# Kernel tuning notes

Hardware: AMD Instinct MI355X
Metric: run time of the kernel (lower is better)

## Reference

```python
import jax, jax.numpy as jnp
import numpy as np

K_SIZE = 32768   # knowledge_size
H = 1024         # hidden_size
Q = 512          # query_dim


def setup_inputs() -> dict:
    key = jax.random.key(0)
    kq, kb_, kwk, kbk, kwv, kbv = jax.random.split(key, 6)
    queries = jax.random.normal(kq, (4, 2048, Q), dtype=jnp.float32)
    knowledge_bank = jax.random.normal(kb_, (K_SIZE, H), dtype=jnp.float32)
    # Linear layers: torch Linear weight [out, in]; we store transposed [in, out]
    lim_k = 1.0 / np.sqrt(H)
    Wk = jax.random.uniform(kwk, (H, Q), jnp.float32, -lim_k, lim_k)
    bk = jax.random.uniform(kbk, (Q,), jnp.float32, -lim_k, lim_k)
    Wv = jax.random.uniform(kwv, (H, H), jnp.float32, -lim_k, lim_k)
    bv = jax.random.uniform(kbv, (H,), jnp.float32, -lim_k, lim_k)
    return {"queries": queries, "knowledge_bank": knowledge_bank,
            "Wk": Wk, "bk": bk, "Wv": Wv, "bv": bv}


def reference(queries, knowledge_bank, Wk, bk, Wv, bv):
    # keys: [K, Q]
    knowledge_keys = knowledge_bank @ Wk + bk
    # scores: [B, S, K]  (note: original applies NO 1/sqrt(d) scaling)
    scores = jnp.einsum('bsq,kq->bsk', queries, knowledge_keys)
    attention = jax.nn.softmax(scores, axis=-1)
    # values: [K, H]
    knowledge_values = knowledge_bank @ Wv + bv
    # retrieved: [B, S, H]
    return jnp.einsum('bsk,kh->bsh', attention, knowledge_values)
```

## Files before the change

### kernel.cpp

```cpp
#include <hip/hip_runtime.h>
#include <cstdint>
#include <cstddef>


typedef __bf16 bf16_t;
typedef __bf16 bf16x4 __attribute__((ext_vector_type(4)));
typedef __bf16 bf16x8 __attribute__((ext_vector_type(8)));
typedef _Float16 f16_t;
typedef _Float16 f16x4 __attribute__((ext_vector_type(4)));
typedef _Float16 f16x8 __attribute__((ext_vector_type(8)));
typedef float f32x4 __attribute__((ext_vector_type(4)));

#define KS   32768
#define HDIM 1024
#define QDIM 512
#define NQ   8192
#define SOFTMAX_C 90.0f

__device__ __forceinline__ void async16(const void* g, void* l) {
  __builtin_amdgcn_global_load_lds((const __attribute__((address_space(1))) void*)g,
                                   (__attribute__((address_space(3))) void*)l, 16, 0, 0);
}

__device__ __forceinline__ void barrier_f() {
  asm volatile("" ::: "memory");
  __builtin_amdgcn_s_barrier();
  asm volatile("" ::: "memory");
}

template <typename T>
__device__ __forceinline__ void stage_tile(const T* gbase, size_t ld, int k0,
                                           T* lds, int wave, int lane) {
  const int gp = ((lane & 3) ^ ((lane >> 3) & 3)) * 8;
  for (int c = wave; c < 8; c += 4) {
    const T* g = gbase + (size_t)(c * 16 + (lane >> 2)) * ld + (size_t)k0 + gp;
    async16((const void*)g, (void*)(lds + c * 512));
  }
}

template <typename T>
__device__ __forceinline__ void stage_half(const T* gbase, size_t ld, int gk,
                                           T* ldsbase, int wave, int lane) {
#pragma unroll
  for (int g = 0; g < 2; ++g) {
    const int slot = g * 512 + wave * 64 + lane;
    const int row = slot >> 2;
    const int cx = (slot & 3) ^ ((row >> 1) & 3);
    const T* src = gbase + (size_t)row * ld + (size_t)gk + cx * 8;
    async16((const void*)src, (void*)(ldsbase + g * 4096 + wave * 512));
  }
}

struct MF16 {
  typedef f16_t T; typedef f16x8 V8;
  static __device__ __forceinline__ f32x4 mm(V8 a, V8 b, f32x4 c) {
    return __builtin_amdgcn_mfma_f32_16x16x32_f16(a, b, c, 0, 0, 0);
  }
};
struct MBF16 {
  typedef bf16_t T; typedef bf16x8 V8;
  static __device__ __forceinline__ f32x4 mm(V8 a, V8 b, f32x4 c) {
    return __builtin_amdgcn_mfma_f32_16x16x32_bf16(a, b, c, 0, 0, 0);
  }
};

template <class M>
__device__ __forceinline__ void gemm256_8p(
    const typename M::T* __restrict__ A, size_t lda,
    const typename M::T* __restrict__ B, size_t ldb,
    int kbeg, int ktiles, typename M::T* sm,
    f32x4 (&acc)[8][4], int wave, int lane) {
  typedef typename M::T T;
  typedef typename M::V8 V8;
  const int wm = wave & 1, wn = wave >> 1;
  const int qd = lane >> 4, ln = lane & 15;
  const int arow = wm * 128 + ln;
  const int brow = wn * 64 + ln;
  const int cxr = (qd ^ ((ln >> 1) & 3)) * 8;

  stage_half(B, ldb, kbeg +  0, sm + 16384, wave, lane);
  stage_half(B, ldb, kbeg + 32, sm + 24576, wave, lane);
  stage_half(A, lda, kbeg +  0, sm +     0, wave, lane);
  stage_half(A, lda, kbeg + 32, sm +  8192, wave, lane);
  stage_half(B, ldb, kbeg + 64, sm + 32768 + 16384, wave, lane);
  stage_half(B, ldb, kbeg + 96, sm + 32768 + 24576, wave, lane);
  stage_half(A, lda, kbeg + 64, sm + 32768, wave, lane);
  asm volatile("s_waitcnt vmcnt(6)" ::: "memory");
  barrier_f();

  V8 ar[4], br0[4], br1[4];
  for (int t = 0; t < ktiles; ++t) {
    const int b = t & 1;
    T* bufA = sm + b * 32768;
    T* bufB = bufA + 16384;
    T* obufA = sm + (b ^ 1) * 32768;
    const int kt = kbeg + t * 64;
#pragma unroll
    for (int j = 0; j < 4; ++j) br0[j] = *(const V8*)&bufB[(brow + j * 16) * 32 + cxr];
#pragma unroll
    for (int i = 0; i < 4; ++i) ar[i] = *(const V8*)&bufA[(arow + i * 16) * 32 + cxr];
    if (t + 1 < ktiles) stage_half(A, lda, kt + 96, obufA + 8192, wave, lane);
    barrier_f();
    asm volatile("s_waitcnt lgkmcnt(0)" ::: "memory");
    __builtin_amdgcn_s_setprio(1);
#pragma unroll
    for (int i = 0; i < 4; ++i)
#pragma unroll
      for (int j = 0; j < 4; ++j) acc[i][j] = M::mm(ar[i], br0[j], acc[i][j]);
    __builtin_amdgcn_s_setprio(0);
    barrier_f();
#pragma unroll
    for (int j = 0; j < 4; ++j) br1[j] = *(const V8*)&bufB[8192 + (brow + j * 16) * 32 + cxr];
#pragma unroll
    for (int i = 0; i < 4; ++i) ar[i] = *(const V8*)&bufA[8192 + (arow + i * 16) * 32 + cxr];
    if (t + 2 < ktiles) stage_half(B, ldb, kt + 128, bufB, wave, lane);
    barrier_f();
    asm volatile("s_waitcnt lgkmcnt(0)" ::: "memory");
    __builtin_amdgcn_s_setprio(1);
#pragma unroll
    for (int i = 0; i < 4; ++i)
#pragma unroll
      for (int j = 0; j < 4; ++j) acc[i][j] = M::mm(ar[i], br1[j], acc[i][j]);
    __builtin_amdgcn_s_setprio(0);
    barrier_f();
#pragma unroll
    for (int i = 0; i < 4; ++i) ar[i] = *(const V8*)&bufA[(arow + 64 + i * 16) * 32 + cxr];
    if (t + 2 < ktiles) stage_half(B, ldb, kt + 160, bufB + 8192, wave, lane);
    barrier_f();
    asm volatile("s_waitcnt lgkmcnt(0)" ::: "memory");
    __builtin_amdgcn_s_setprio(1);
#pragma unroll
    for (int i = 0; i < 4; ++i)
#pragma unroll
      for (int j = 0; j < 4; ++j) acc[4 + i][j] = M::mm(ar[i], br0[j], acc[4 + i][j]);
    __builtin_amdgcn_s_setprio(0);
    barrier_f();
#pragma unroll
    for (int i = 0; i < 4; ++i) ar[i] = *(const V8*)&bufA[8192 + (arow + 64 + i * 16) * 32 + cxr];
    if (t + 2 < ktiles) stage_half(A, lda, kt + 128, bufA, wave, lane);
    barrier_f();
    asm volatile("s_waitcnt lgkmcnt(0)" ::: "memory");
    __builtin_amdgcn_s_setprio(1);
#pragma unroll
    for (int i = 0; i < 4; ++i)
#pragma unroll
      for (int j = 0; j < 4; ++j) acc[4 + i][j] = M::mm(ar[i], br1[j], acc[4 + i][j]);
    __builtin_amdgcn_s_setprio(0);
    if (t + 2 < ktiles) { asm volatile("s_waitcnt vmcnt(6)" ::: "memory"); }
    else                { asm volatile("s_waitcnt vmcnt(0)" ::: "memory"); }
    barrier_f();
  }
}

__global__ __launch_bounds__(256) void prep_q(const float* __restrict__ q,
                                              f16_t* __restrict__ qf) {
  int g = blockIdx.x * 256 + threadIdx.x;
  float4 v = *(const float4*)(q + (size_t)g * 4);
  f16x4 h;
  h[0] = (f16_t)v.x; h[1] = (f16_t)v.y; h[2] = (f16_t)v.z; h[3] = (f16_t)v.w;
  *(f16x4*)(qf + (size_t)g * 4) = h;
}

__global__ __launch_bounds__(256) void prep_bank(const float* __restrict__ bank,
                                                 f16_t* __restrict__ bh,
                                                 bf16_t* __restrict__ bb) {
  size_t g = (size_t)blockIdx.x * 256 + threadIdx.x;
  float4 v = *(const float4*)(bank + g * 4);
  f16x4 h;
  h[0] = (f16_t)v.x; h[1] = (f16_t)v.y; h[2] = (f16_t)v.z; h[3] = (f16_t)v.w;
  *(f16x4*)(bh + g * 4) = h;
  bf16x4 b;
  b[0] = (bf16_t)v.x; b[1] = (bf16_t)v.y; b[2] = (bf16_t)v.z; b[3] = (bf16_t)v.w;
  *(bf16x4*)(bb + g * 4) = b;
}

__global__ __launch_bounds__(256) void prep_wk(const float* __restrict__ Wk,
                                               f16_t* __restrict__ WkTf) {
  int t = blockIdx.x * 256 + threadIdx.x;
  int n = t >> 10, k = t & 1023;
  WkTf[t] = (f16_t)Wk[(size_t)k * QDIM + n];
}

__global__ __launch_bounds__(256) void prep_wv(const float* __restrict__ Wv,
                                               bf16_t* __restrict__ WvT) {
  int t = blockIdx.x * 256 + threadIdx.x;
  int n = t >> 10, k = t & 1023;
  WvT[t] = (bf16_t)(Wv[(size_t)k * HDIM + n]);
}

__global__ __launch_bounds__(256) void keys_gemm(const f16_t* __restrict__ bh,
                                                 const f16_t* __restrict__ WkTf,
                                                 const float* __restrict__ bk,
                                                 f16_t* __restrict__ kf) {
  __shared__ alignas(16) f16_t lA[128 * 32];
  __shared__ alignas(16) f16_t lB[128 * 32];
  const int tid = threadIdx.x, lane = tid & 63, wave = tid >> 6;
  const int wm = wave & 1, wn = wave >> 1;
  const int qd = lane >> 4, ln = lane & 15;
  const int m0 = blockIdx.y * 128;
  const int n0 = blockIdx.x * 128;
  const int kqs = ((qd ^ ((ln >> 1) & 3)) << 3);
  f32x4 acc[4][4] = {};
  for (int k0 = 0; k0 < HDIM; k0 += 32) {
    stage_tile(bh + (size_t)m0 * HDIM, HDIM, k0, lA, wave, lane);
    stage_tile(WkTf + (size_t)n0 * HDIM, HDIM, k0, lB, wave, lane);
    __syncthreads();
    f16x8 af[4], bfr[4];
#pragma unroll
    for (int i = 0; i < 4; i++)
      af[i] = *(const f16x8*)&lA[(wm * 64 + i * 16 + ln) * 32 + kqs];
#pragma unroll
    for (int j = 0; j < 4; j++)
      bfr[j] = *(const f16x8*)&lB[(wn * 64 + j * 16 + ln) * 32 + kqs];
#pragma unroll
    for (int i = 0; i < 4; i++)
#pragma unroll
      for (int j = 0; j < 4; j++)
        acc[i][j] = __builtin_amdgcn_mfma_f32_16x16x32_f16(af[i], bfr[j], acc[i][j], 0, 0, 0);
    __syncthreads();
  }
#pragma unroll
  for (int j = 0; j < 4; j++) {
    const int cc = n0 + wn * 64 + j * 16 + ln;
    const float bkc = bk[cc];
#pragma unroll
    for (int i = 0; i < 4; i++) {
      const int rr = m0 + wm * 64 + i * 16 + qd * 4;
#pragma unroll
      for (int r = 0; r < 4; r++)
        kf[(size_t)(rr + r) * QDIM + cc] = (f16_t)(acc[i][j][r] + bkc);
    }
  }
}

__global__ __launch_bounds__(256) void values_gemm_t(const bf16_t* __restrict__ bb,
                                                     const bf16_t* __restrict__ WvT,
                                                     const float* __restrict__ bv,
                                                     bf16_t* __restrict__ VT) {
  __shared__ alignas(16) bf16_t lA[128 * 32];
  __shared__ alignas(16) bf16_t lB[128 * 32];
  const int tid = threadIdx.x, lane = tid & 63, wave = tid >> 6;
  const int wm = wave & 1, wn = wave >> 1;
  const int qd = lane >> 4, ln = lane & 15;
  const int m0 = blockIdx.x * 128;
  const int n0 = blockIdx.y * 128;
  const int kqs = ((qd ^ ((ln >> 1) & 3)) << 3);
  f32x4 acc[4][4] = {};
  for (int k0 = 0; k0 < HDIM; k0 += 32) {
    stage_tile(WvT + (size_t)m0 * HDIM, HDIM, k0, lA, wave, lane);
    stage_tile(bb + (size_t)n0 * HDIM, HDIM, k0, lB, wave, lane);
    __syncthreads();
    bf16x8 af[4], bfr[4];
#pragma unroll
    for (int i = 0; i < 4; i++)
      af[i] = *(const bf16x8*)&lA[(wm * 64 + i * 16 + ln) * 32 + kqs];
#pragma unroll
    for (int j = 0; j < 4; j++)
      bfr[j] = *(const bf16x8*)&lB[(wn * 64 + j * 16 + ln) * 32 + kqs];
#pragma unroll
    for (int i = 0; i < 4; i++)
#pragma unroll
      for (int j = 0; j < 4; j++)
        acc[i][j] = __builtin_amdgcn_mfma_f32_16x16x32_bf16(af[i], bfr[j], acc[i][j], 0, 0, 0);
    __syncthreads();
  }
#pragma unroll
  for (int i = 0; i < 4; i++) {
#pragma unroll
    for (int r = 0; r < 4; r++) {
      const int hh = m0 + wm * 64 + i * 16 + qd * 4 + r;
      const float bvc = bv[hh];
#pragma unroll
      for (int j = 0; j < 4; j++) {
        const int cc = n0 + wn * 64 + j * 16 + ln;
        VT[(size_t)hh * KS + cc] = (bf16_t)(acc[i][j][r] + bvc);
      }
    }
  }
}

__global__ __launch_bounds__(512, 2) void score_fused_8p(
    const f16_t* __restrict__ qf, const f16_t* __restrict__ kf,
    bf16_t* __restrict__ P, float* __restrict__ lpart, int row0, int mtiles) {
  __shared__ alignas(16) f16_t sm[65536];
  const int tid = threadIdx.x, lane = tid & 63, wave = tid >> 6;
  const int bid = blockIdx.x;
  const int logical = (bid & 7) * ((int)gridDim.x >> 3) + (bid >> 3);
  const int mt_ = logical % mtiles;
  const int nt_ = logical / mtiles;
  const int m0 = mt_ * 256, n0 = nt_ * 256;
  f32x4 acc[8][4] = {};
  gemm256_8p<MF16>(qf + (size_t)(row0 + m0) * QDIM, QDIM,
                   kf + (size_t)n0 * QDIM, QDIM, 0, QDIM / 64, sm, acc, wave, lane);

  const int wm = wave & 1, wn = wave >> 1;
  const int qd = lane >> 4, ln = lane & 15;
  float* ls = (float*)sm;
  if (tid < 256) ls[tid] = 0.f;
  __syncthreads();
  float rsum[8][4];
#pragma unroll
  for (int ii = 0; ii < 8; ++ii) {
    const int rr = m0 + wm * 128 + ii * 16 + qd * 4;
#pragma unroll
    for (int r = 0; r < 4; ++r) rsum[ii][r] = 0.f;
#pragma unroll
    for (int j = 0; j < 4; ++j) {
      const int cc = n0 + wn * 64 + j * 16 + ln;
#pragma unroll
      for (int r = 0; r < 4; ++r) {
        float e = __expf(acc[ii][j][r] - SOFTMAX_C);
        bf16_t pb = (bf16_t)e;
        P[(size_t)(rr + r) * KS + cc] = pb;
        rsum[ii][r] += (float)pb;
      }
    }
  }
#pragma unroll
  for (int ii = 0; ii < 8; ++ii)
#pragma unroll
    for (int r = 0; r < 4; ++r) {
      float s = rsum[ii][r];
#pragma unroll
      for (int off = 1; off < 16; off <<= 1) s += __shfl_xor(s, off);
      if (ln == 0) atomicAdd(&ls[wm * 128 + ii * 16 + qd * 4 + r], s);
    }
  __syncthreads();
  if (tid < 256)
    lpart[(size_t)(row0 + m0 + tid) * (KS / 256) + nt_] = ls[tid];
}

__global__ __launch_bounds__(512, 2) void pv_gemm_8p(
    const bf16_t* __restrict__ P, const bf16_t* __restrict__ VT,
    float* __restrict__ Out, int row0, int mtiles) {
  __shared__ alignas(16) bf16_t sm[65536];
  const int tid = threadIdx.x, lane = tid & 63, wave = tid >> 6;
  const int bid = blockIdx.x;
  const int z = bid & 7;
  const int idx = bid >> 3;
  const int mt_ = idx % mtiles;
  const int nt_ = idx / mtiles;
  const int m0 = mt_ * 256;
  const int n0 = nt_ * 256;
  const int kbeg = z * (KS / 8);
  f32x4 acc[8][4] = {};
  gemm256_8p<MBF16>(P + (size_t)m0 * KS, KS,
                    VT + (size_t)n0 * KS, KS, kbeg, (KS / 8) / 64, sm, acc, wave, lane);

  const int wm = wave & 1, wn = wave >> 1;
  const int qd = lane >> 4, ln = lane & 15;
#pragma unroll
  for (int j = 0; j < 4; ++j) {
    const int cc = n0 + wn * 64 + j * 16 + ln;
#pragma unroll
    for (int ii = 0; ii < 8; ++ii) {
      const int rb = m0 + wm * 128 + ii * 16 + qd * 4;
#pragma unroll
      for (int r = 0; r < 4; ++r)
        atomicAdd(Out + (size_t)(row0 + rb + r) * HDIM + cc, acc[ii][j][r]);
    }
  }
}

__global__ __launch_bounds__(256) void normalize(const float* __restrict__ lpart,
                                                 float* __restrict__ Out) {
  const int row = blockIdx.x;
  float s = (threadIdx.x < 128) ? lpart[(size_t)row * 128 + threadIdx.x] : 0.f;
#pragma unroll
  for (int off = 32; off; off >>= 1) s += __shfl_xor(s, off);
  __shared__ float red[4];
  if ((threadIdx.x & 63) == 0) red[threadIdx.x >> 6] = s;
  __syncthreads();
  const float linv = 1.0f / (red[0] + red[1] + red[2] + red[3]);
  float4* o = (float4*)(Out + (size_t)row * HDIM) + threadIdx.x;
  float4 v = *o;
  v.x *= linv; v.y *= linv; v.z *= linv; v.w *= linv;
  *o = v;
}

extern "C" void kernel_launch(void* const* d_in, const int* in_sizes, int n_in,
                              void* d_out, int out_size, void* d_ws, size_t ws_size,
                              hipStream_t stream) {
  const float* q    = (const float*)d_in[0];
  const float* bank = (const float*)d_in[1];
  const float* Wk   = (const float*)d_in[2];
  const float* bk   = (const float*)d_in[3];
  const float* Wv   = (const float*)d_in[4];
  const float* bv   = (const float*)d_in[5];
  float* out = (float*)d_out;
  char* ws = (char*)d_ws;

  size_t off = 0;
  f16_t*  qf    = (f16_t*)(ws + off);  off += (size_t)NQ * QDIM * 2;
  f16_t*  kf    = (f16_t*)(ws + off);  off += (size_t)KS * QDIM * 2;
  bf16_t* VT    = (bf16_t*)(ws + off); off += (size_t)HDIM * KS * 2;
  f16_t*  bkf16 = (f16_t*)(ws + off);  off += (size_t)KS * HDIM * 2;
  bf16_t* bkbf  = (bf16_t*)(ws + off); off += (size_t)KS * HDIM * 2;
  f16_t*  wkf   = (f16_t*)(ws + off);  off += (size_t)QDIM * HDIM * 2;
  bf16_t* wvt   = (bf16_t*)(ws + off); off += (size_t)HDIM * HDIM * 2;
  float*  lpart = (float*)(ws + off);  off += (size_t)NQ * 256 * 4;

  int R = 2048;
  while (R > 256 && off + (size_t)R * KS * 2 > ws_size) R >>= 1;
  bf16_t* P = (bf16_t*)(ws + off);
  const int Rm = R / 256;

  hipMemsetAsync(d_out, 0, (size_t)out_size * sizeof(float), stream);

  prep_q   <<<NQ * QDIM / 4 / 256, 256, 0, stream>>>(q, qf);
  prep_bank<<<KS * HDIM / 4 / 256, 256, 0, stream>>>(bank, bkf16, bkbf);
  prep_wk  <<<QDIM * HDIM / 256, 256, 0, stream>>>(Wk, wkf);
  prep_wv  <<<HDIM * HDIM / 256, 256, 0, stream>>>(Wv, wvt);
  keys_gemm    <<<dim3(QDIM / 128, KS / 128), 256, 0, stream>>>(bkf16, wkf, bk, kf);
  values_gemm_t<<<dim3(HDIM / 128, KS / 128), 256, 0, stream>>>(bkbf, wvt, bv, VT);

  for (int row0 = 0; row0 < NQ; row0 += R) {
    score_fused_8p<<<(KS / 256) * Rm, 512, 0, stream>>>(qf, kf, P, lpart, row0, Rm);
    pv_gemm_8p    <<<8 * Rm * (HDIM / 256), 512, 0, stream>>>(P, VT, out, row0, Rm);
  }
  normalize<<<NQ, 256, 0, stream>>>(lpart, out);
}
```

Before: 1.449 ms.

## Replace atomic split-K output with slab partials and fused reduce-normalize; trim GEMM barriers

The PV GEMM now writes each K-split's partial tile into a scratch slab instead of issuing fp32 atomicAdds to the output. A new per-chunk reduce kernel sums the slabs and applies the softmax normalization, which also removes the output memset. The split count scales with chunk size R. Separately, the GEMM main loop drops three barriers and the explicit lgkmcnt waits and moves the last MFMA block after the final barrier, to cut synchronization stalls. This relies on the compiler inserting the LDS read waits and on reusing the bank fp16 buffer as slab storage, and the extra slab traffic adds memory cost.

```diff
diff --git a/kernel.cpp b/kernel.cpp
--- a/kernel.cpp
+++ b/kernel.cpp
@@ -101,54 +101,46 @@
     for (int i = 0; i < 4; ++i) ar[i] = *(const V8*)&bufA[(arow + i * 16) * 32 + cxr];
     if (t + 1 < ktiles) stage_half(A, lda, kt + 96, obufA + 8192, wave, lane);
     barrier_f();
-    asm volatile("s_waitcnt lgkmcnt(0)" ::: "memory");
     __builtin_amdgcn_s_setprio(1);
 #pragma unroll
     for (int i = 0; i < 4; ++i)
 #pragma unroll
       for (int j = 0; j < 4; ++j) acc[i][j] = M::mm(ar[i], br0[j], acc[i][j]);
     __builtin_amdgcn_s_setprio(0);
-    barrier_f();
 #pragma unroll
     for (int j = 0; j < 4; ++j) br1[j] = *(const V8*)&bufB[8192 + (brow + j * 16) * 32 + cxr];
 #pragma unroll
     for (int i = 0; i < 4; ++i) ar[i] = *(const V8*)&bufA[8192 + (arow + i * 16) * 32 + cxr];
     if (t + 2 < ktiles) stage_half(B, ldb, kt + 128, bufB, wave, lane);
     barrier_f();
-    asm volatile("s_waitcnt lgkmcnt(0)" ::: "memory");
     __builtin_amdgcn_s_setprio(1);
 #pragma unroll
     for (int i = 0; i < 4; ++i)
 #pragma unroll
       for (int j = 0; j < 4; ++j) acc[i][j] = M::mm(ar[i], br1[j], acc[i][j]);
     __builtin_amdgcn_s_setprio(0);
-    barrier_f();
 #pragma unroll
     for (int i = 0; i < 4; ++i) ar[i] = *(const V8*)&bufA[(arow + 64 + i * 16) * 32 + cxr];
     if (t + 2 < ktiles) stage_half(B, ldb, kt + 160, bufB + 8192, wave, lane);
     barrier_f();
-    asm volatile("s_waitcnt lgkmcnt(0)" ::: "memory");
     __builtin_amdgcn_s_setprio(1);
 #pragma unroll
     for (int i = 0; i < 4; ++i)
 #pragma unroll
       for (int j = 0; j < 4; ++j) acc[4 + i][j] = M::mm(ar[i], br0[j], acc[4 + i][j]);
     __builtin_amdgcn_s_setprio(0);
-    barrier_f();
 #pragma unroll
     for (int i = 0; i < 4; ++i) ar[i] = *(const V8*)&bufA[8192 + (arow + 64 + i * 16) * 32 + cxr];
     if (t + 2 < ktiles) stage_half(A, lda, kt + 128, bufA, wave, lane);
-    barrier_f();
-    asm volatile("s_waitcnt lgkmcnt(0)" ::: "memory");
-    __builtin_amdgcn_s_setprio(1);
-#pragma unroll
-    for (int i = 0; i < 4; ++i)
-#pragma unroll
-      for (int j = 0; j < 4; ++j) acc[4 + i][j] = M::mm(ar[i], br1[j], acc[4 + i][j]);
-    __builtin_amdgcn_s_setprio(0);
     if (t + 2 < ktiles) { asm volatile("s_waitcnt vmcnt(6)" ::: "memory"); }
     else                { asm volatile("s_waitcnt vmcnt(0)" ::: "memory"); }
     barrier_f();
+    __builtin_amdgcn_s_setprio(1);
+#pragma unroll
+    for (int i = 0; i < 4; ++i)
+#pragma unroll
+      for (int j = 0; j < 4; ++j) acc[4 + i][j] = M::mm(ar[i], br1[j], acc[4 + i][j]);
+    __builtin_amdgcn_s_setprio(0);
   }
 }
 
@@ -332,23 +324,25 @@
 
 __global__ __launch_bounds__(512, 2) void pv_gemm_8p(
     const bf16_t* __restrict__ P, const bf16_t* __restrict__ VT,
-    float* __restrict__ Out, int row0, int mtiles) {
+    float* __restrict__ slab, int mtiles, int zsplit) {
   __shared__ alignas(16) bf16_t sm[65536];
   const int tid = threadIdx.x, lane = tid & 63, wave = tid >> 6;
   const int bid = blockIdx.x;
-  const int z = bid & 7;
-  const int idx = bid >> 3;
+  const int z = bid % zsplit;
+  const int idx = bid / zsplit;
   const int mt_ = idx % mtiles;
   const int nt_ = idx / mtiles;
   const int m0 = mt_ * 256;
   const int n0 = nt_ * 256;
-  const int kbeg = z * (KS / 8);
+  const int kspan = KS / zsplit;
+  const int kbeg = z * kspan;
   f32x4 acc[8][4] = {};
   gemm256_8p<MBF16>(P + (size_t)m0 * KS, KS,
-                    VT + (size_t)n0 * KS, KS, kbeg, (KS / 8) / 64, sm, acc, wave, lane);
+                    VT + (size_t)n0 * KS, KS, kbeg, kspan / 64, sm, acc, wave, lane);
 
   const int wm = wave & 1, wn = wave >> 1;
   const int qd = lane >> 4, ln = lane & 15;
+  float* slabz = slab + (size_t)z * (size_t)(mtiles * 256) * HDIM;
 #pragma unroll
   for (int j = 0; j < 4; ++j) {
     const int cc = n0 + wn * 64 + j * 16 + ln;
@@ -357,25 +351,31 @@
       const int rb = m0 + wm * 128 + ii * 16 + qd * 4;
 #pragma unroll
       for (int r = 0; r < 4; ++r)
-        atomicAdd(Out + (size_t)(row0 + rb + r) * HDIM + cc, acc[ii][j][r]);
+        slabz[(size_t)(rb + r) * HDIM + cc] = acc[ii][j][r];
     }
   }
 }
 
-__global__ __launch_bounds__(256) void normalize(const float* __restrict__ lpart,
-                                                 float* __restrict__ Out) {
+__global__ __launch_bounds__(256) void reduce_norm(const float* __restrict__ slab,
+                                                   const float* __restrict__ lpart,
+                                                   float* __restrict__ Out,
+                                                   int row0, int R, int zsplit) {
   const int row = blockIdx.x;
-  float s = (threadIdx.x < 128) ? lpart[(size_t)row * 128 + threadIdx.x] : 0.f;
+  float s = (threadIdx.x < 128) ? lpart[(size_t)(row0 + row) * (KS / 256) + threadIdx.x] : 0.f;
 #pragma unroll
   for (int off = 32; off; off >>= 1) s += __shfl_xor(s, off);
   __shared__ float red[4];
   if ((threadIdx.x & 63) == 0) red[threadIdx.x >> 6] = s;
   __syncthreads();
   const float linv = 1.0f / (red[0] + red[1] + red[2] + red[3]);
-  float4* o = (float4*)(Out + (size_t)row * HDIM) + threadIdx.x;
-  float4 v = *o;
-  v.x *= linv; v.y *= linv; v.z *= linv; v.w *= linv;
-  *o = v;
+  const float* p = slab + (size_t)row * HDIM + threadIdx.x * 4;
+  float4 a = make_float4(0.f, 0.f, 0.f, 0.f);
+  for (int zz = 0; zz < zsplit; ++zz) {
+    float4 v = *(const float4*)(p + (size_t)zz * R * HDIM);
+    a.x += v.x; a.y += v.y; a.z += v.z; a.w += v.w;
+  }
+  a.x *= linv; a.y *= linv; a.z *= linv; a.w *= linv;
+  *(float4*)(Out + (size_t)(row0 + row) * HDIM + threadIdx.x * 4) = a;
 }
 
 extern "C" void kernel_launch(void* const* d_in, const int* in_sizes, int n_in,
@@ -405,7 +405,10 @@
   bf16_t* P = (bf16_t*)(ws + off);
   const int Rm = R / 256;
 
-  hipMemsetAsync(d_out, 0, (size_t)out_size * sizeof(float), stream);
+  int zsplit = 16384 / R;
+  if (zsplit < 8) zsplit = 8;
+  if (zsplit > 64) zsplit = 64;
+  float* slab = (float*)bkf16;
 
   prep_q   <<<NQ * QDIM / 4 / 256, 256, 0, stream>>>(q, qf);
   prep_bank<<<KS * HDIM / 4 / 256, 256, 0, stream>>>(bank, bkf16, bkbf);
@@ -416,7 +419,7 @@
 
   for (int row0 = 0; row0 < NQ; row0 += R) {
     score_fused_8p<<<(KS / 256) * Rm, 512, 0, stream>>>(qf, kf, P, lpart, row0, Rm);
-    pv_gemm_8p    <<<8 * Rm * (HDIM / 256), 512, 0, stream>>>(P, VT, out, row0, Rm);
-  }
-  normalize<<<NQ, 256, 0, stream>>>(lpart, out);
-}
+    pv_gemm_8p    <<<zsplit * Rm * (HDIM / 256), 512, 0, stream>>>(P, VT, slab, Rm, zsplit);
+    reduce_norm   <<<R, 256, 0, stream>>>(slab, lpart, out, row0, R, zsplit);
+  }
+}
```

After: 1.367 ms. -5.7%, faster.
